# Kernel tuning notes

Measured on AMD Instinct MI355X. Metric: run time of the kernel, lower is better.

## Reference

```python
import jax, jax.numpy as jnp
import numpy as np

N_NODES = 20000
N_EDGES = 320000
IN_CH = 64
OUT_CH = 128

def _gat(x, src, dst, W, a_src, a_dst, bias, concat):
    # PyG GATConv: linear -> per-edge leaky_relu attention logits -> segment softmax over dst -> scatter-weighted sum
    N = x.shape[0]
    H, C = a_src.shape
    xl = (x @ W).reshape(N, H, C)                       # [N,H,C]
    al = (xl * a_src).sum(-1)                           # [N,H] src logits
    ar = (xl * a_dst).sum(-1)                           # [N,H] dst logits
    e = jax.nn.leaky_relu(al[src] + ar[dst], 0.2)       # [E,H]
    emax = jax.ops.segment_max(e, dst, num_segments=N)  # every node has a self loop -> no empty segments
    ee = jnp.exp(e - emax[dst])
    denom = jax.ops.segment_sum(ee, dst, num_segments=N)
    alpha = ee / (denom[dst] + 1e-16)                   # [E,H]
    out = jax.ops.segment_sum(xl[src] * alpha[:, :, None], dst, num_segments=N)  # [N,H,C]
    out = out.reshape(N, H * C) if concat else out.mean(axis=1)
    return out + bias

def setup_inputs() -> dict:
    key = jax.random.key(0)
    ks = jax.random.split(key, 32)
    def lin(k, fi, fo):
        return jax.random.normal(k, (fi, fo), jnp.float32) / np.sqrt(fi)
    def att(k, H, C):
        return jax.random.normal(k, (H, C), jnp.float32) / np.sqrt(C)
    x = jax.random.normal(ks[0], (N_NODES, IN_CH), jnp.float32)
    src = jax.random.randint(ks[1], (N_EDGES,), 0, N_NODES, jnp.int32)
    dst = jax.random.randint(ks[2], (N_EDGES,), 0, N_NODES, jnp.int32)
    dst = jnp.where(dst == src, (dst + 1) % N_NODES, dst)  # avoid pre-existing self loops
    edge_index = jnp.stack([src, dst])
    edge_time = jax.random.uniform(ks[3], (N_EDGES,), jnp.float32)
    H = 4
    return {
        "x": x, "edge_time": edge_time,
        "W1": lin(ks[4], IN_CH, 512), "as1": att(ks[5], H, 128), "ad1": att(ks[6], H, 128), "b1": jnp.zeros((512,), jnp.float32),
        "W2": lin(ks[7], 512, 512),   "as2": att(ks[8], H, 128), "ad2": att(ks[9], H, 128), "b2": jnp.zeros((512,), jnp.float32),
        "W3": lin(ks[10], 512, 512),  "as3": att(ks[11], H, 128), "ad3": att(ks[12], H, 128), "b3": jnp.zeros((OUT_CH,), jnp.float32),
        "tW1": lin(ks[13], 1, 64), "tb1": jnp.zeros((64,), jnp.float32),
        "tW2": lin(ks[14], 64, OUT_CH), "tb2": jnp.zeros((OUT_CH,), jnp.float32),
        "fW1": lin(ks[15], 2 * OUT_CH, OUT_CH), "fb1": jnp.zeros((OUT_CH,), jnp.float32),
        "fW2": lin(ks[16], OUT_CH, OUT_CH), "fb2": jnp.zeros((OUT_CH,), jnp.float32),
        "ln_g": jnp.ones((OUT_CH,), jnp.float32), "ln_b": jnp.zeros((OUT_CH,), jnp.float32),
        "rW": lin(ks[17], IN_CH, OUT_CH), "rb": jnp.zeros((OUT_CH,), jnp.float32),
        "edge_index": edge_index,
    }

def reference(x, edge_time, W1, as1, ad1, b1, W2, as2, ad2, b2, W3, as3, ad3, b3,
              tW1, tb1, tW2, tb2, fW1, fb1, fW2, fb2, ln_g, ln_b, rW, rb, edge_index):
    N = x.shape[0]
    loop = jnp.arange(N, dtype=edge_index.dtype)
    src = jnp.concatenate([edge_index[0], loop])
    dst = jnp.concatenate([edge_index[1], loop])
    # temporal embedding of raw (pre-self-loop) edges
    t = edge_time[:, None]
    time_emb = jax.nn.relu(t @ tW1 + tb1) @ tW2 + tb2    # [E, OUT_CH]
    x_res = x @ rW + rb
    h = jax.nn.relu(_gat(x, src, dst, W1, as1, ad1, b1, True))
    h = jax.nn.relu(_gat(h, src, dst, W2, as2, ad2, b2, True))
    h = jax.nn.relu(_gat(h, src, dst, W3, as3, ad3, b3, False))
    # x_agg[row] += h[col]  with (row, col) = (src, dst) incl. self loops
    agg = jax.ops.segment_sum(h[dst], src, num_segments=N)
    tm = jnp.broadcast_to(time_emb.mean(axis=0)[None, :], (N, time_emb.shape[1]))
    z = jnp.concatenate([agg, tm], axis=1)
    z = jax.nn.relu(z @ fW1 + fb1)                        # dropout is identity in eval
    z = z @ fW2 + fb2
    mu = z.mean(-1, keepdims=True)
    var = ((z - mu) ** 2).mean(-1, keepdims=True)
    z = (z - mu) / jnp.sqrt(var + 1e-5) * ln_g + ln_b
    return z + x_res
```

## Files before the change

kernel.cpp:

```cpp
#include <hip/hip_runtime.h>
#include <hip/hip_bf16.h>
#include <math.h>

typedef short bf16x8 __attribute__((ext_vector_type(8)));
typedef float f32x4 __attribute__((ext_vector_type(4)));

__device__ __forceinline__ float lrelu(float v) { return v > 0.f ? v : 0.2f * v; }

__device__ __forceinline__ void gload16(const void* g, void* l) {
  __builtin_amdgcn_global_load_lds(
      (const __attribute__((address_space(1))) void*)g,
      (__attribute__((address_space(3))) void*)l, 16, 0, 0);
}

__device__ __forceinline__ uint packbf(float v0, float v1) {
  __hip_bfloat16 h0 = __float2bfloat16(v0);
  __hip_bfloat16 h1 = __float2bfloat16(v1);
  return (uint)(*(unsigned short*)&h0) | ((uint)(*(unsigned short*)&h1) << 16);
}

__global__ __launch_bounds__(256) void k_countT(const int* __restrict__ src,
    const int* __restrict__ dst, int E, int* cntD, int* cntS,
    const float* __restrict__ et, const float* __restrict__ tW1,
    const float* __restrict__ tb1, float* __restrict__ tacc) {
  int t = threadIdx.x;
  int e = blockIdx.x * 256 + t;
  if (e < E) {
    atomicAdd(&cntD[dst[e]], 1);
    atomicAdd(&cntS[src[e]], 1);
  }
  if (blockIdx.x < 256) {
    __shared__ float se[256];
    __shared__ float buf[256];
    int l = t & 63, w = t >> 6;
    float wk = tW1[l], bk = tb1[l];
    float a0 = 0.f, a1 = 0.f, a2 = 0.f, a3 = 0.f;
    for (int base = blockIdx.x * 256; base < E; base += 256 * 256) {
      int idx = base + t;
      se[t] = (idx < E) ? et[idx] : 0.f;
      __syncthreads();
      int cnt = E - base; if (cnt > 256) cnt = 256;
      int s0 = w * 64;
      int c = cnt - s0; if (c < 0) c = 0; if (c > 64) c = 64;
      int j = 0;
      for (; j + 4 <= c; j += 4) {
        a0 += fmaxf(se[s0 + j] * wk + bk, 0.f);
        a1 += fmaxf(se[s0 + j + 1] * wk + bk, 0.f);
        a2 += fmaxf(se[s0 + j + 2] * wk + bk, 0.f);
        a3 += fmaxf(se[s0 + j + 3] * wk + bk, 0.f);
      }
      for (; j < c; ++j) a0 += fmaxf(se[s0 + j] * wk + bk, 0.f);
      __syncthreads();
    }
    buf[t] = (a0 + a1) + (a2 + a3);
    __syncthreads();
    if (t < 64) {
      float s = buf[t] + buf[t + 64] + buf[t + 128] + buf[t + 192];
      atomicAdd(&tacc[t], s);
    }
  }
}

__global__ __launch_bounds__(1024) void k_scan2c(const int* __restrict__ cntD, int* __restrict__ offD,
    const int* __restrict__ cntS, int* __restrict__ offS, int n,
    const float* __restrict__ tacc, const float* __restrict__ tW2,
    const float* __restrict__ tb2, const float* __restrict__ fW1,
    const float* __restrict__ fb1, float* __restrict__ cvec, int E) {
  int t = threadIdx.x;
  if (blockIdx.x == 2) {
    __shared__ float tm[128];
    if (t < 128) {
      float inv = 1.f / (float)E;
      float acc = tb2[t];
      for (int k = 0; k < 64; ++k) acc += (tacc[k] * inv) * tW2[k * 128 + t];
      tm[t] = acc;
    }
    __syncthreads();
    if (t < 128) {
      float c = fb1[t];
      for (int k = 0; k < 128; ++k) c += tm[k] * fW1[(128 + k) * 128 + t];
      cvec[t] = c;
    }
    return;
  }
  const int* cnt = blockIdx.x ? cntS : cntD;
  int* off = blockIdx.x ? offS : offD;
  __shared__ int sums[1024];
  int PT = (n + 1023) >> 10;
  int start = t * PT;
  int local = 0;
  for (int i = 0; i < PT; ++i) {
    int idx = start + i;
    if (idx < n) local += cnt[idx];
  }
  sums[t] = local;
  __syncthreads();
  for (int o = 1; o < 1024; o <<= 1) {
    int v = (t >= o) ? sums[t - o] : 0;
    __syncthreads();
    sums[t] += v;
    __syncthreads();
  }
  int run = sums[t] - local;
  for (int i = 0; i < PT; ++i) {
    int idx = start + i;
    if (idx < n) { off[idx] = run; run += cnt[idx]; }
  }
  if (t == 1023) off[n] = run;
}

__global__ void k_fill(const int* __restrict__ src, const int* __restrict__ dst, int E,
                       const int* __restrict__ offD, int* curD, int* lstD,
                       const int* __restrict__ offS, int* curS, int* lstS) {
  int e = blockIdx.x * blockDim.x + threadIdx.x;
  if (e < E) {
    int d = dst[e], s = src[e];
    int p = atomicAdd(&curD[d], 1);
    lstD[offD[d] + p] = s;
    int q = atomicAdd(&curS[s], 1);
    lstS[offS[s] + q] = d;
  }
}

struct PrepArgs {
  const float* W[6]; __hip_bfloat16* Wt[6]; int K[6]; int Nw[6]; int tstart[6];
  int NC, XB;
};

__global__ __launch_bounds__(256) void k_prep(PrepArgs a, const float* __restrict__ x,
    __hip_bfloat16* __restrict__ xbf, __hip_bfloat16* __restrict__ habf,
    __hip_bfloat16* __restrict__ aggbf, int N, int Mp) {
  __shared__ float tile[32][65];
  int bid = blockIdx.x;
  int t = threadIdx.x;
  if (bid < a.NC) {
    int m = 0;
#pragma unroll
    for (int i = 1; i < 6; ++i) if (bid >= a.tstart[i]) m = i;
    const float* W = a.W[m];
    __hip_bfloat16* Wt = a.Wt[m];
    int K = a.K[m], Nw = a.Nw[m];
    int lt = bid - a.tstart[m];
    int ntn = Nw >> 6;
    int bk = (lt / ntn) * 32, bn = (lt % ntn) * 64;
    int rn = t & 63, rk = t >> 6;
#pragma unroll
    for (int i = 0; i < 8; ++i)
      tile[rk + i * 4][rn] = W[(size_t)(bk + rk + i * 4) * Nw + bn + rn];
    __syncthreads();
    int wk2 = (t & 15) * 2, wn = t >> 4;
    uint* Wo = (uint*)Wt;
#pragma unroll
    for (int i = 0; i < 4; ++i) {
      int n = wn + i * 16;
      Wo[((size_t)(bn + n) * K + bk + wk2) >> 1] = packbf(tile[wk2][n], tile[wk2 + 1][n]);
    }
  } else if (bid < a.NC + a.XB) {
    int i4 = (bid - a.NC) * 256 + t;
    int row = i4 >> 4;
    float4 v = make_float4(0.f, 0.f, 0.f, 0.f);
    if (row < N) v = ((const float4*)x)[i4];
    uint2 p; p.x = packbf(v.x, v.y); p.y = packbf(v.z, v.w);
    ((uint2*)xbf)[i4] = p;
  } else {
    int row = N + (bid - a.NC - a.XB);
    ((uint*)habf)[(size_t)row * 256 + t] = 0;
    if (t < 64) ((uint*)aggbf)[(size_t)row * 64 + t] = 0;
  }
}

template<int EPI>
__global__ __launch_bounds__(256) void gemm_t(
    const __hip_bfloat16* __restrict__ A, const __hip_bfloat16* __restrict__ Bt,
    void* __restrict__ Cout, const float* __restrict__ bias,
    int M, int Nw, int K, int relu, int Nn,
    const float* __restrict__ asrc, const float* __restrict__ adst,
    float* __restrict__ al, float* __restrict__ ar,
    float* __restrict__ C2, const float* __restrict__ bias2,
    const float* __restrict__ lng, const float* __restrict__ lnb,
    float* __restrict__ resid)
{
  __shared__ short As0[128 * 32];
  __shared__ short As1[128 * 32];
  __shared__ short Bs0[128 * 32];
  __shared__ short Bs1[128 * 32];
  int tid = threadIdx.x;
  int bm = blockIdx.x * 128;
  int cb = blockIdx.y;
  int bn = cb * 128;
  int w = tid >> 6, l = tid & 63;
  int wr = (w >> 1) * 64, wc = (w & 1) * 64;
  f32x4 acc[4][4] = {};
  const short* Ag = (const short*)A;
  const short* Bg = (const short*)Bt;

  for (int k0 = 0; k0 < K; k0 += 64) {
#pragma unroll
    for (int i = 0; i < 2; ++i) {
      int slot = i * 256 + tid;
      int row = slot >> 2;
      int col = (slot & 3) * 8;
      const short* Arow = Ag + (size_t)(bm + row) * K + k0 + col;
      const short* Brow = Bg + (size_t)(bn + row) * K + k0 + col;
      gload16(Arow, &As0[slot * 8]);
      gload16(Arow + 32, &As1[slot * 8]);
      gload16(Brow, &Bs0[slot * 8]);
      gload16(Brow + 32, &Bs1[slot * 8]);
    }
    __syncthreads();
    {
      bf16x8 af[4], bfr[4];
#pragma unroll
      for (int m = 0; m < 4; ++m)
        af[m] = *(const bf16x8*)&As0[(wr + m * 16 + (l & 15)) * 32 + (l >> 4) * 8];
#pragma unroll
      for (int n = 0; n < 4; ++n)
        bfr[n] = *(const bf16x8*)&Bs0[(wc + n * 16 + (l & 15)) * 32 + (l >> 4) * 8];
#pragma unroll
      for (int m = 0; m < 4; ++m)
#pragma unroll
        for (int n = 0; n < 4; ++n)
          acc[m][n] = __builtin_amdgcn_mfma_f32_16x16x32_bf16(af[m], bfr[n], acc[m][n], 0, 0, 0);
    }
    {
      bf16x8 af[4], bfr[4];
#pragma unroll
      for (int m = 0; m < 4; ++m)
        af[m] = *(const bf16x8*)&As1[(wr + m * 16 + (l & 15)) * 32 + (l >> 4) * 8];
#pragma unroll
      for (int n = 0; n < 4; ++n)
        bfr[n] = *(const bf16x8*)&Bs1[(wc + n * 16 + (l & 15)) * 32 + (l >> 4) * 8];
#pragma unroll
      for (int m = 0; m < 4; ++m)
#pragma unroll
        for (int n = 0; n < 4; ++n)
          acc[m][n] = __builtin_amdgcn_mfma_f32_16x16x32_bf16(af[m], bfr[n], acc[m][n], 0, 0, 0);
    }
    __syncthreads();
  }

  int g = l >> 4, cc = l & 15, cr = g * 4;

  if (EPI == 0) {
#pragma unroll
    for (int n = 0; n < 4; ++n) {
      int col = bn + wc + n * 16 + cc;
      float bb = bias ? bias[col] : 0.f;
#pragma unroll
      for (int m = 0; m < 4; ++m) {
#pragma unroll
        for (int r = 0; r < 4; ++r) {
          int gm = bm + wr + m * 16 + cr + r;
          if (gm < M) {
            float v = acc[m][n][r] + bb;
            if (relu) v = fmaxf(v, 0.f);
            ((__hip_bfloat16*)Cout)[(size_t)gm * Nw + col] = __float2bfloat16(v);
          }
        }
      }
    }
  }

  if (EPI == 1) {
    if (cb < 4) {
#pragma unroll
      for (int n = 0; n < 4; ++n) {
        int col = bn + wc + n * 16 + cc;
#pragma unroll
        for (int m = 0; m < 4; ++m) {
#pragma unroll
          for (int r = 0; r < 4; ++r) {
            int gm = bm + wr + m * 16 + cr + r;
            if (gm < M)
              ((__hip_bfloat16*)Cout)[(size_t)gm * 512 + col] = __float2bfloat16(acc[m][n][r]);
          }
        }
      }
      float asv[4], adv[4];
#pragma unroll
      for (int n = 0; n < 4; ++n) {
        int ch = bn + wc + n * 16 + cc;
        asv[n] = asrc[ch]; adv[n] = adst[ch];
      }
      float* spal = (float*)As0;
      float* spar = spal + 256;
#pragma unroll
      for (int m = 0; m < 4; ++m) {
#pragma unroll
        for (int r = 0; r < 4; ++r) {
          float pa = acc[m][0][r] * asv[0] + acc[m][1][r] * asv[1]
                   + acc[m][2][r] * asv[2] + acc[m][3][r] * asv[3];
          float pb = acc[m][0][r] * adv[0] + acc[m][1][r] * adv[1]
                   + acc[m][2][r] * adv[2] + acc[m][3][r] * adv[3];
#pragma unroll
          for (int o = 1; o < 16; o <<= 1) {
            pa += __shfl_xor(pa, o);
            pb += __shfl_xor(pb, o);
          }
          if (cc == 0) {
            int rl = m * 16 + cr + r;
            spal[w * 64 + rl] = pa;
            spar[w * 64 + rl] = pb;
          }
        }
      }
      __syncthreads();
      if ((w & 1) == 0) {
        float av = spal[w * 64 + l] + spal[(w + 1) * 64 + l];
        float rv = spar[w * 64 + l] + spar[(w + 1) * 64 + l];
        int row = bm + wr + l;
        if (row < Nn) { al[row * 4 + cb] = av; ar[row * 4 + cb] = rv; }
      }
    } else {
#pragma unroll
      for (int n = 0; n < 4; ++n) {
        int col2 = wc + n * 16 + cc;
        float bb = bias2[col2];
#pragma unroll
        for (int m = 0; m < 4; ++m) {
#pragma unroll
          for (int r = 0; r < 4; ++r) {
            int gm = bm + wr + m * 16 + cr + r;
            if (gm < Nn) C2[(size_t)gm * 128 + col2] = acc[m][n][r] + bb;
          }
        }
      }
    }
  }

  if (EPI == 2) {
    float bb[4], gl_[4], gb_[4];
#pragma unroll
    for (int n = 0; n < 4; ++n) {
      int col = wc + n * 16 + cc;
      bb[n] = bias[col]; gl_[n] = lng[col]; gb_[n] = lnb[col];
    }
    float* ssum = (float*)As0;
    float* ssq = ssum + 256;
    float* smu = ssum + 512;
    float* srs = ssum + 640;
#pragma unroll
    for (int m = 0; m < 4; ++m) {
#pragma unroll
      for (int r = 0; r < 4; ++r) {
        float s = 0.f, q = 0.f;
#pragma unroll
        for (int n = 0; n < 4; ++n) {
          float z = acc[m][n][r] + bb[n];
          s += z; q += z * z;
        }
#pragma unroll
        for (int o = 1; o < 16; o <<= 1) {
          s += __shfl_xor(s, o);
          q += __shfl_xor(q, o);
        }
        if (cc == 0) {
          int rl = m * 16 + cr + r;
          ssum[w * 64 + rl] = s;
          ssq[w * 64 + rl] = q;
        }
      }
    }
    __syncthreads();
    if ((w & 1) == 0) {
      float s = ssum[w * 64 + l] + ssum[(w + 1) * 64 + l];
      float q = ssq[w * 64 + l] + ssq[(w + 1) * 64 + l];
      float mu = s * (1.f / 128.f);
      float var = q * (1.f / 128.f) - mu * mu;
      smu[wr + l] = mu;
      srs[wr + l] = rsqrtf(var + 1e-5f);
    }
    __syncthreads();
#pragma unroll
    for (int m = 0; m < 4; ++m) {
#pragma unroll
      for (int r = 0; r < 4; ++r) {
        int rl = wr + m * 16 + cr + r;
        int gm = bm + rl;
        if (gm < M) {
          float mu = smu[rl], rs = srs[rl];
#pragma unroll
          for (int n = 0; n < 4; ++n) {
            int col = wc + n * 16 + cc;
            float z = acc[m][n][r] + bb[n];
            float y = (z - mu) * rs * gl_[n] + gb_[n] + resid[(size_t)gm * 128 + col];
            resid[(size_t)gm * 128 + col] = y;
          }
        }
      }
    }
  }
}

__global__ __launch_bounds__(256) void k_gat_agg(
    const __hip_bfloat16* __restrict__ xl, const float* __restrict__ al,
    const float* __restrict__ ar, const int* __restrict__ off,
    const int* __restrict__ lst, const float* __restrict__ bias,
    __hip_bfloat16* __restrict__ outb, __hip_bfloat16* __restrict__ outh,
    int mode, int N)
{
  __shared__ int   sside[4][64];
  __shared__ float sebuf[4][4][68];
  int w = threadIdx.x >> 6, l = threadIdx.x & 63;
  int d = blockIdx.x * 4 + w;
  bool active = (d < N);
  int base = 0, deg = 0, tot = 0;
  float4 arv = make_float4(0.f, 0.f, 0.f, 0.f);
  if (active) {
    base = off[d]; deg = off[d + 1] - base; tot = deg + 1;
    arv = *(const float4*)(ar + 4 * d);
  }
  int hh = l >> 4;
  float facc[8] = {0.f, 0.f, 0.f, 0.f, 0.f, 0.f, 0.f, 0.f};
  float dn0 = 0.f, dn1 = 0.f, dn2 = 0.f, dn3 = 0.f;
  const uint4* xw = (const uint4*)xl;
  auto fma8 = [&](uint4 pv, float e) {
    facc[0] += e * __uint_as_float(pv.x << 16);
    facc[1] += e * __uint_as_float(pv.x & 0xffff0000u);
    facc[2] += e * __uint_as_float(pv.y << 16);
    facc[3] += e * __uint_as_float(pv.y & 0xffff0000u);
    facc[4] += e * __uint_as_float(pv.z << 16);
    facc[5] += e * __uint_as_float(pv.z & 0xffff0000u);
    facc[6] += e * __uint_as_float(pv.w << 16);
    facc[7] += e * __uint_as_float(pv.w & 0xffff0000u);
  };
  for (int cb = 0; cb < tot; cb += 64) {
    int j = cb + l;
    float e0 = 0.f, e1 = 0.f, e2 = 0.f, e3 = 0.f;
    int sid = 0;
    if (j < tot) {
      sid = (j == deg) ? d : lst[base + j];
      float4 av = *(const float4*)(al + 4 * sid);
      e0 = __expf(lrelu(av.x + arv.x));
      e1 = __expf(lrelu(av.y + arv.y));
      e2 = __expf(lrelu(av.z + arv.z));
      e3 = __expf(lrelu(av.w + arv.w));
      dn0 += e0; dn1 += e1; dn2 += e2; dn3 += e3;
    }
    sside[w][l] = sid;
    sebuf[w][0][l] = e0; sebuf[w][1][l] = e1;
    sebuf[w][2][l] = e2; sebuf[w][3][l] = e3;
    int cnt = tot - cb; if (cnt > 64) cnt = 64;
    int jj = 0;
    for (; jj + 4 <= cnt; jj += 4) {
      int s0 = sside[w][jj], s1 = sside[w][jj + 1];
      int s2 = sside[w][jj + 2], s3 = sside[w][jj + 3];
      float ea = sebuf[w][hh][jj], eb = sebuf[w][hh][jj + 1];
      float ec = sebuf[w][hh][jj + 2], ed = sebuf[w][hh][jj + 3];
      uint4 p0 = xw[(size_t)s0 * 64 + l];
      uint4 p1 = xw[(size_t)s1 * 64 + l];
      uint4 p2 = xw[(size_t)s2 * 64 + l];
      uint4 p3 = xw[(size_t)s3 * 64 + l];
      fma8(p0, ea); fma8(p1, eb); fma8(p2, ec); fma8(p3, ed);
    }
    for (; jj < cnt; ++jj) {
      int s0 = sside[w][jj];
      float ea = sebuf[w][hh][jj];
      uint4 p0 = xw[(size_t)s0 * 64 + l];
      fma8(p0, ea);
    }
  }
#pragma unroll
  for (int o = 1; o < 64; o <<= 1) {
    dn0 += __shfl_xor(dn0, o); dn1 += __shfl_xor(dn1, o);
    dn2 += __shfl_xor(dn2, o); dn3 += __shfl_xor(dn3, o);
  }
  if (!active) return;
  float dsel = hh == 0 ? dn0 : hh == 1 ? dn1 : hh == 2 ? dn2 : dn3;
  float rden = 1.f / dsel;
  if (mode == 0) {
    int c8 = l * 8;
    const float4* bp = (const float4*)(bias + c8);
    float4 b0 = bp[0], b1 = bp[1];
    float vb[8] = {b0.x, b0.y, b0.z, b0.w, b1.x, b1.y, b1.z, b1.w};
    uint4 o4; uint* po = (uint*)&o4;
#pragma unroll
    for (int i = 0; i < 4; ++i) {
      float v0 = fmaxf(facc[2*i]   * rden + vb[2*i],   0.f);
      float v1 = fmaxf(facc[2*i+1] * rden + vb[2*i+1], 0.f);
      po[i] = packbf(v0, v1);
    }
    ((uint4*)outb)[(size_t)d * 64 + l] = o4;
  } else {
#pragma unroll
    for (int i = 0; i < 8; ++i) {
      facc[i] *= rden;
      facc[i] += __shfl_xor(facc[i], 16);
      facc[i] += __shfl_xor(facc[i], 32);
    }
    if (l < 16) {
      int c = l * 8;
      const float4* bp = (const float4*)(bias + c);
      float4 b0 = bp[0], b1 = bp[1];
      float vb[8] = {b0.x, b0.y, b0.z, b0.w, b1.x, b1.y, b1.z, b1.w};
      uint4 o4; uint* po = (uint*)&o4;
#pragma unroll
      for (int i = 0; i < 4; ++i) {
        float v0 = fmaxf(facc[2*i]   * 0.25f + vb[2*i],   0.f);
        float v1 = fmaxf(facc[2*i+1] * 0.25f + vb[2*i+1], 0.f);
        po[i] = packbf(v0, v1);
      }
      ((uint4*)outh)[(size_t)d * 16 + l] = o4;
    }
  }
}

__global__ __launch_bounds__(256) void k_aggsrc(const __hip_bfloat16* __restrict__ h3,
    const int* __restrict__ off, const int* __restrict__ lst,
    __hip_bfloat16* __restrict__ out, int N) {
  int w = threadIdx.x >> 6, l = threadIdx.x & 63;
  int n = blockIdx.x * 4 + w;
  if (n >= N) return;
  const uint* hw = (const uint*)h3;
  uint pv = hw[(size_t)n * 64 + l];
  float a0 = __uint_as_float(pv << 16);
  float a1 = __uint_as_float(pv & 0xffff0000u);
  float b0 = 0.f, b1 = 0.f, c0 = 0.f, c1 = 0.f, d0 = 0.f, d1 = 0.f;
  int b = off[n], e = off[n + 1];
  int j = b;
  for (; j + 4 <= e; j += 4) {
    int s0 = lst[j], s1 = lst[j + 1], s2 = lst[j + 2], s3 = lst[j + 3];
    uint q0 = hw[(size_t)s0 * 64 + l];
    uint q1 = hw[(size_t)s1 * 64 + l];
    uint q2 = hw[(size_t)s2 * 64 + l];
    uint q3 = hw[(size_t)s3 * 64 + l];
    a0 += __uint_as_float(q0 << 16); a1 += __uint_as_float(q0 & 0xffff0000u);
    b0 += __uint_as_float(q1 << 16); b1 += __uint_as_float(q1 & 0xffff0000u);
    c0 += __uint_as_float(q2 << 16); c1 += __uint_as_float(q2 & 0xffff0000u);
    d0 += __uint_as_float(q3 << 16); d1 += __uint_as_float(q3 & 0xffff0000u);
  }
  for (; j < e; ++j) {
    uint q = hw[(size_t)lst[j] * 64 + l];
    a0 += __uint_as_float(q << 16);
    a1 += __uint_as_float(q & 0xffff0000u);
  }
  ((uint*)out)[(size_t)n * 64 + l] = packbf((a0 + b0) + (c0 + d0), (a1 + b1) + (c1 + d1));
}

extern "C" void kernel_launch(void* const* d_in, const int* in_sizes, int n_in,
                              void* d_out, int out_size, void* d_ws, size_t ws_size,
                              hipStream_t stream) {
  (void)n_in; (void)out_size; (void)ws_size;
  const float* x   = (const float*)d_in[0];
  const float* et  = (const float*)d_in[1];
  const float* W1  = (const float*)d_in[2];
  const float* as1 = (const float*)d_in[3];
  const float* ad1 = (const float*)d_in[4];
  const float* b1  = (const float*)d_in[5];
  const float* W2  = (const float*)d_in[6];
  const float* as2 = (const float*)d_in[7];
  const float* ad2 = (const float*)d_in[8];
  const float* b2  = (const float*)d_in[9];
  const float* W3  = (const float*)d_in[10];
  const float* as3 = (const float*)d_in[11];
  const float* ad3 = (const float*)d_in[12];
  const float* b3  = (const float*)d_in[13];
  const float* tW1 = (const float*)d_in[14];
  const float* tb1 = (const float*)d_in[15];
  const float* tW2 = (const float*)d_in[16];
  const float* tb2 = (const float*)d_in[17];
  const float* fW1 = (const float*)d_in[18];
  const float* fb1 = (const float*)d_in[19];
  const float* fW2 = (const float*)d_in[20];
  const float* fb2 = (const float*)d_in[21];
  const float* lng = (const float*)d_in[22];
  const float* lnb = (const float*)d_in[23];
  const float* rW  = (const float*)d_in[24];
  const float* rb  = (const float*)d_in[25];
  const int*   ei  = (const int*)d_in[26];
  const int N = in_sizes[0] / 64;
  const int E = in_sizes[26] / 2;
  const int Mp = ((N + 127) / 128) * 128;
  const int* src = ei;
  const int* dst = ei + E;

  char* cur = (char*)d_ws;
  auto carve = [&](size_t bytes) { char* p = cur; cur += (bytes + 255) & ~(size_t)255; return p; };
  __hip_bfloat16* xbf  = (__hip_bfloat16*)carve((size_t)Mp * 64 * 2);
  __hip_bfloat16* habf = (__hip_bfloat16*)carve((size_t)Mp * 512 * 2);
  __hip_bfloat16* xlbf = (__hip_bfloat16*)carve((size_t)Mp * 512 * 2);
  __hip_bfloat16* wtCat= (__hip_bfloat16*)carve((size_t)640 * 64 * 2);
  __hip_bfloat16* wt2  = (__hip_bfloat16*)carve((size_t)512 * 512 * 2);
  __hip_bfloat16* wt3  = (__hip_bfloat16*)carve((size_t)512 * 512 * 2);
  __hip_bfloat16* wtF1 = (__hip_bfloat16*)carve((size_t)128 * 128 * 2);
  __hip_bfloat16* wtF2 = (__hip_bfloat16*)carve((size_t)128 * 128 * 2);
  __hip_bfloat16* aggbf= (__hip_bfloat16*)carve((size_t)Mp * 128 * 2);
  __hip_bfloat16* z1bf = (__hip_bfloat16*)carve((size_t)Mp * 128 * 2);
  __hip_bfloat16* h3   = (__hip_bfloat16*)carve((size_t)N * 128 * 2);
  float* al   = (float*)carve((size_t)N * 4 * 4);
  float* ar   = (float*)carve((size_t)N * 4 * 4);
  float* cvec = (float*)carve(128 * 4);
  int* offD = (int*)carve((size_t)(N + 1) * 4);
  int* offS = (int*)carve((size_t)(N + 1) * 4);
  int* lstD = (int*)carve((size_t)E * 4);
  int* lstS = (int*)carve((size_t)E * 4);
  char* zstart = cur;
  int* cntD = (int*)carve((size_t)N * 4);
  int* curD = (int*)carve((size_t)N * 4);
  int* cntS = (int*)carve((size_t)N * 4);
  int* curS = (int*)carve((size_t)N * 4);
  float* tacc = (float*)carve(64 * 4);
  size_t zbytes = (size_t)(cur - zstart);
  float* xres = (float*)d_out;

  hipMemsetAsync(zstart, 0, zbytes, stream);

  k_countT<<<(E + 255) / 256, 256, 0, stream>>>(src, dst, E, cntD, cntS, et, tW1, tb1, tacc);
  k_scan2c<<<3, 1024, 0, stream>>>(cntD, offD, cntS, offS, N, tacc, tW2, tb2, fW1, fb1, cvec, E);
  k_fill<<<(E + 255) / 256, 256, 0, stream>>>(src, dst, E, offD, curD, lstD, offS, curS, lstS);

  {
    PrepArgs pa;
    int ts = 0;
    auto setd = [&](int i, const float* W, __hip_bfloat16* Wt, int K, int Nw) {
      pa.W[i] = W; pa.Wt[i] = Wt; pa.K[i] = K; pa.Nw[i] = Nw; pa.tstart[i] = ts;
      ts += (K / 32) * (Nw / 64);
    };
    setd(0, W1, wtCat, 64, 512);
    setd(1, W2, wt2, 512, 512);
    setd(2, W3, wt3, 512, 512);
    setd(3, rW, wtCat + (size_t)512 * 64, 64, 128);
    setd(4, fW1, wtF1, 128, 128);
    setd(5, fW2, wtF2, 128, 128);
    pa.NC = ts;
    pa.XB = Mp / 16;
    int grid = pa.NC + pa.XB + (Mp - N);
    k_prep<<<grid, 256, 0, stream>>>(pa, x, xbf, habf, aggbf, N, Mp);
  }

  const int TB = Mp / 128;
  const int GB = (N + 3) / 4;

  gemm_t<1><<<dim3(TB, 5), 256, 0, stream>>>(xbf, wtCat, xlbf, nullptr, Mp, 640, 64, 0, N,
      as1, ad1, al, ar, xres, rb, nullptr, nullptr, nullptr);
  k_gat_agg<<<GB, 256, 0, stream>>>(xlbf, al, ar, offD, lstD, b1, habf, nullptr, 0, N);
  gemm_t<1><<<dim3(TB, 4), 256, 0, stream>>>(habf, wt2, xlbf, nullptr, Mp, 512, 512, 0, N,
      as2, ad2, al, ar, nullptr, nullptr, nullptr, nullptr, nullptr);
  k_gat_agg<<<GB, 256, 0, stream>>>(xlbf, al, ar, offD, lstD, b2, habf, nullptr, 0, N);
  gemm_t<1><<<dim3(TB, 4), 256, 0, stream>>>(habf, wt3, xlbf, nullptr, Mp, 512, 512, 0, N,
      as3, ad3, al, ar, nullptr, nullptr, nullptr, nullptr, nullptr);
  k_gat_agg<<<GB, 256, 0, stream>>>(xlbf, al, ar, offD, lstD, b3, nullptr, h3, 1, N);

  k_aggsrc<<<GB, 256, 0, stream>>>(h3, offS, lstS, aggbf, N);

  gemm_t<0><<<dim3(TB, 1), 256, 0, stream>>>(aggbf, wtF1, z1bf, cvec, Mp, 128, 128, 1, N,
      nullptr, nullptr, nullptr, nullptr, nullptr, nullptr, nullptr, nullptr, nullptr);
  gemm_t<2><<<dim3(TB, 1), 256, 0, stream>>>(z1bf, wtF2, nullptr, fb2, N, 128, 128, 0, N,
      nullptr, nullptr, nullptr, nullptr, nullptr, nullptr, lng, lnb, xres);
}
```

Baseline: 380.4 us.

## Split concat GAT aggregation into per-column-phase blocks for higher parallelism

For the two concat GAT layers, a new kernel launches 8x more blocks, each handling a 64-column slice (half a head) of the 512-wide output per destination node. Two half-waves split the edges, and each lane reads a 4-byte word instead of a 16-byte vector. The aim is more blocks in flight and a smaller per-block working set, so the irregular gather latency is better hidden. In exchange, the edge lists and attention logits are re-read and the exponentials recomputed 8 times, and each gather access is narrower. The final mean-head layer keeps the original kernel, with the concat mode removed from it.

```diff
diff --git a/kernel.cpp b/kernel.cpp
--- a/kernel.cpp
+++ b/kernel.cpp
@@ -392,12 +392,80 @@
   }
 }
 
+__global__ __launch_bounds__(256) void k_gat_phase(
+    const __hip_bfloat16* __restrict__ xl, const float* __restrict__ al,
+    const float* __restrict__ ar, const int* __restrict__ off,
+    const int* __restrict__ lst, const float* __restrict__ bias,
+    __hip_bfloat16* __restrict__ outb, int GB, int N)
+{
+  __shared__ int   sside[4][64];
+  __shared__ float sebuf[4][64];
+  int w = threadIdx.x >> 6, l = threadIdx.x & 63;
+  int ph = blockIdx.x / GB;
+  int bx = blockIdx.x - ph * GB;
+  int h = ph >> 1;
+  int d = bx * 4 + w;
+  bool active = (d < N);
+  int base = 0, deg = 0, tot = 0;
+  float arh = 0.f;
+  if (active) {
+    base = off[d]; deg = off[d + 1] - base; tot = deg + 1;
+    arh = ar[4 * d + h];
+  }
+  int hl = l & 31;
+  int eh = l >> 5;
+  float f0 = 0.f, f1 = 0.f;
+  float dn = 0.f;
+  const uint* xw = (const uint*)xl;
+  int uoff = ph * 32 + hl;
+  for (int cb = 0; cb < tot; cb += 64) {
+    int j = cb + l;
+    float e = 0.f;
+    int sid = 0;
+    if (j < tot) {
+      sid = (j == deg) ? d : lst[base + j];
+      e = __expf(lrelu(al[4 * sid + h] + arh));
+      dn += e;
+    }
+    sside[w][l] = sid;
+    sebuf[w][l] = e;
+    int cnt = tot - cb; if (cnt > 64) cnt = 64;
+    int jj = eh;
+    for (; jj + 2 < cnt; jj += 4) {
+      int s0 = sside[w][jj], s1 = sside[w][jj + 2];
+      float e0 = sebuf[w][jj], e1 = sebuf[w][jj + 2];
+      uint p0 = xw[(size_t)s0 * 256 + uoff];
+      uint p1 = xw[(size_t)s1 * 256 + uoff];
+      f0 += e0 * __uint_as_float(p0 << 16);
+      f1 += e0 * __uint_as_float(p0 & 0xffff0000u);
+      f0 += e1 * __uint_as_float(p1 << 16);
+      f1 += e1 * __uint_as_float(p1 & 0xffff0000u);
+    }
+    for (; jj < cnt; jj += 2) {
+      int s0 = sside[w][jj];
+      float e0 = sebuf[w][jj];
+      uint p0 = xw[(size_t)s0 * 256 + uoff];
+      f0 += e0 * __uint_as_float(p0 << 16);
+      f1 += e0 * __uint_as_float(p0 & 0xffff0000u);
+    }
+  }
+#pragma unroll
+  for (int o = 1; o < 64; o <<= 1) dn += __shfl_xor(dn, o);
+  f0 += __shfl_xor(f0, 32);
+  f1 += __shfl_xor(f1, 32);
+  if (!active || eh) return;
+  float rden = 1.f / dn;
+  int c0 = ph * 64 + hl * 2;
+  float v0 = fmaxf(f0 * rden + bias[c0], 0.f);
+  float v1 = fmaxf(f1 * rden + bias[c0 + 1], 0.f);
+  ((uint*)outb)[(size_t)d * 256 + uoff] = packbf(v0, v1);
+}
+
 __global__ __launch_bounds__(256) void k_gat_agg(
     const __hip_bfloat16* __restrict__ xl, const float* __restrict__ al,
     const float* __restrict__ ar, const int* __restrict__ off,
     const int* __restrict__ lst, const float* __restrict__ bias,
-    __hip_bfloat16* __restrict__ outb, __hip_bfloat16* __restrict__ outh,
-    int mode, int N)
+    __hip_bfloat16* __restrict__ outh, int N)
 {
   __shared__ int   sside[4][64];
   __shared__ float sebuf[4][4][68];
@@ -468,40 +536,25 @@
   if (!active) return;
   float dsel = hh == 0 ? dn0 : hh == 1 ? dn1 : hh == 2 ? dn2 : dn3;
   float rden = 1.f / dsel;
-  if (mode == 0) {
-    int c8 = l * 8;
-    const float4* bp = (const float4*)(bias + c8);
+#pragma unroll
+  for (int i = 0; i < 8; ++i) {
+    facc[i] *= rden;
+    facc[i] += __shfl_xor(facc[i], 16);
+    facc[i] += __shfl_xor(facc[i], 32);
+  }
+  if (l < 16) {
+    int c = l * 8;
+    const float4* bp = (const float4*)(bias + c);
     float4 b0 = bp[0], b1 = bp[1];
     float vb[8] = {b0.x, b0.y, b0.z, b0.w, b1.x, b1.y, b1.z, b1.w};
     uint4 o4; uint* po = (uint*)&o4;
 #pragma unroll
     for (int i = 0; i < 4; ++i) {
-      float v0 = fmaxf(facc[2*i]   * rden + vb[2*i],   0.f);
-      float v1 = fmaxf(facc[2*i+1] * rden + vb[2*i+1], 0.f);
+      float v0 = fmaxf(facc[2*i]   * 0.25f + vb[2*i],   0.f);
+      float v1 = fmaxf(facc[2*i+1] * 0.25f + vb[2*i+1], 0.f);
       po[i] = packbf(v0, v1);
     }
-    ((uint4*)outb)[(size_t)d * 64 + l] = o4;
-  } else {
-#pragma unroll
-    for (int i = 0; i < 8; ++i) {
-      facc[i] *= rden;
-      facc[i] += __shfl_xor(facc[i], 16);
-      facc[i] += __shfl_xor(facc[i], 32);
-    }
-    if (l < 16) {
-      int c = l * 8;
-      const float4* bp = (const float4*)(bias + c);
-      float4 b0 = bp[0], b1 = bp[1];
-      float vb[8] = {b0.x, b0.y, b0.z, b0.w, b1.x, b1.y, b1.z, b1.w};
-      uint4 o4; uint* po = (uint*)&o4;
-#pragma unroll
-      for (int i = 0; i < 4; ++i) {
-        float v0 = fmaxf(facc[2*i]   * 0.25f + vb[2*i],   0.f);
-        float v1 = fmaxf(facc[2*i+1] * 0.25f + vb[2*i+1], 0.f);
-        po[i] = packbf(v0, v1);
-      }
-      ((uint4*)outh)[(size_t)d * 16 + l] = o4;
-    }
+    ((uint4*)outh)[(size_t)d * 16 + l] = o4;
   }
 }
 
@@ -633,13 +686,13 @@
 
   gemm_t<1><<<dim3(TB, 5), 256, 0, stream>>>(xbf, wtCat, xlbf, nullptr, Mp, 640, 64, 0, N,
       as1, ad1, al, ar, xres, rb, nullptr, nullptr, nullptr);
-  k_gat_agg<<<GB, 256, 0, stream>>>(xlbf, al, ar, offD, lstD, b1, habf, nullptr, 0, N);
+  k_gat_phase<<<GB * 8, 256, 0, stream>>>(xlbf, al, ar, offD, lstD, b1, habf, GB, N);
   gemm_t<1><<<dim3(TB, 4), 256, 0, stream>>>(habf, wt2, xlbf, nullptr, Mp, 512, 512, 0, N,
       as2, ad2, al, ar, nullptr, nullptr, nullptr, nullptr, nullptr);
-  k_gat_agg<<<GB, 256, 0, stream>>>(xlbf, al, ar, offD, lstD, b2, habf, nullptr, 0, N);
+  k_gat_phase<<<GB * 8, 256, 0, stream>>>(xlbf, al, ar, offD, lstD, b2, habf, GB, N);
   gemm_t<1><<<dim3(TB, 4), 256, 0, stream>>>(habf, wt3, xlbf, nullptr, Mp, 512, 512, 0, N,
       as3, ad3, al, ar, nullptr, nullptr, nullptr, nullptr, nullptr);
-  k_gat_agg<<<GB, 256, 0, stream>>>(xlbf, al, ar, offD, lstD, b3, nullptr, h3, 1, N);
+  k_gat_agg<<<GB, 256, 0, stream>>>(xlbf, al, ar, offD, lstD, b3, h3, N);
 
   k_aggsrc<<<GB, 256, 0, stream>>>(h3, offS, lstS, aggbf, N);
 
```

Result: slower. 449.9 us (+18.3%).
